# Performance work log

Measured on AMD Instinct MI355X. Metric: run time of the kernel, lower is better.

## Reference

```python
import jax, jax.numpy as jnp
import numpy as np

N_STEPS = 5


def setup_inputs() -> dict:
    key = jax.random.key(0)
    ks = jax.random.split(key, 12)
    B, N, E, D = 4, 2048, 2, 128
    prop_state = jax.random.normal(ks[0], (B, N, D), dtype=jnp.float32)
    A = (jax.random.uniform(ks[1], (B, N, 2 * N * E)) < 0.01).astype(jnp.float32)
    s = 0.02  # init scale from _initialization
    W_in = jax.random.normal(ks[2], (E, D, D), dtype=jnp.float32) * s
    b_in = jax.random.normal(ks[3], (E, D), dtype=jnp.float32) * s
    W_out = jax.random.normal(ks[4], (E, D, D), dtype=jnp.float32) * s
    b_out = jax.random.normal(ks[5], (E, D), dtype=jnp.float32) * s
    W_r = jax.random.normal(ks[6], (3 * D, D), dtype=jnp.float32) * s
    b_r = jax.random.normal(ks[7], (D,), dtype=jnp.float32) * s
    W_z = jax.random.normal(ks[8], (3 * D, D), dtype=jnp.float32) * s
    b_z = jax.random.normal(ks[9], (D,), dtype=jnp.float32) * s
    W_h = jax.random.normal(ks[10], (3 * D, D), dtype=jnp.float32) * s
    b_h = jax.random.normal(ks[11], (D,), dtype=jnp.float32) * s
    return {"prop_state": prop_state, "A": A, "W_in": W_in, "b_in": b_in,
            "W_out": W_out, "b_out": b_out, "W_r": W_r, "b_r": b_r,
            "W_z": W_z, "b_z": b_z, "W_h": W_h, "b_h": b_h}


def _ggnn_forward(prop_state, A, W_in, b_in, W_out, b_out,
                  W_r, b_r, W_z, b_z, W_h, b_h):
    B, N, D = prop_state.shape
    E = W_in.shape[0]
    A_in = A[:, :, : N * E]    # [B, N, N*E]
    A_out = A[:, :, N * E:]    # [B, N, N*E]
    h = prop_state
    for _ in range(N_STEPS):
        # per-edge-type projections, node-major / edge-type-minor ordering
        ins = (jnp.einsum('bnd,edf->bnef', h, W_in) + b_in).reshape(B, N * E, D)
        outs = (jnp.einsum('bnd,edf->bnef', h, W_out) + b_out).reshape(B, N * E, D)
        a_in = jnp.einsum('bnm,bmd->bnd', A_in, ins)    # [B, N, D]
        a_out = jnp.einsum('bnm,bmd->bnd', A_out, outs)  # [B, N, D]
        a = jnp.concatenate([a_in, a_out, h], axis=-1)   # [B, N, 3D]
        r = jax.nn.sigmoid(a @ W_r + b_r)
        z = jax.nn.sigmoid(a @ W_z + b_z)
        joined = jnp.concatenate([a_in, a_out, r * h], axis=-1)
        h_hat = jnp.tanh(joined @ W_h + b_h)
        h = (1.0 - z) * h + z * h_hat
    return h


def reference(prop_state, A, W_in, b_in, W_out, b_out,
              W_r, b_r, W_z, b_z, W_h, b_h):
    return _ggnn_forward(prop_state, A, W_in, b_in, W_out, b_out,
                         W_r, b_r, W_z, b_z, W_h, b_h)
```

## Files before the change

kernel.cpp:

```cpp
#include <hip/hip_runtime.h>
#include <stdint.h>

#define ROWS 8192
#define CAP 64
#define NSTEPS 5
#define ZROW 8192

typedef short bf16x8 __attribute__((ext_vector_type(8)));
typedef float f32x4 __attribute__((ext_vector_type(4)));
typedef float f32x2 __attribute__((ext_vector_type(2)));
typedef unsigned short u16;
typedef unsigned int u32;

__device__ __forceinline__ float bf2f(u16 u){ union{u32 i; float f;} x; x.i=(u32)u<<16; return x.f; }
__device__ __forceinline__ u16 f2bf(float f){ union{float f; u32 i;} x; x.f=f; u32 r = x.i + 0x7fffu + ((x.i>>16)&1u); return (u16)(r>>16); }

#define MFMA __builtin_amdgcn_mfma_f32_16x16x32_bf16
#define SWZ(r, byte) ((byte) ^ (((r)&7)<<4))
#define ZPAD 130


__device__ __forceinline__ float wsel(const float* __restrict__ Wr, const float* __restrict__ Wz,
                                      const float* __restrict__ Wh, int f, int o){
  if (o < 128) return Wr[(size_t)f*128 + o];
  if (o < 256) return Wz[(size_t)f*128 + (o-128)];
  return (f < 256) ? Wh[(size_t)f*128 + (o-256)] : 0.f;
}

__global__ void k_prep(const float* __restrict__ prop, float* __restrict__ hf, u16* __restrict__ hbf,
                       const float* __restrict__ W_in, const float* __restrict__ b_in,
                       const float* __restrict__ W_out, const float* __restrict__ b_out,
                       const float* __restrict__ W_r, const float* __restrict__ W_z,
                       const float* __restrict__ W_h,
                       u16* __restrict__ WfT, float* __restrict__ bv, u16* __restrict__ WhbT)
{
  int bid = blockIdx.x;
  if (bid < 4096){
    int i = bid*256 + threadIdx.x;
    float v = prop[i]; hf[i] = v; hbf[i] = f2bf(v);
    return;
  }
  if (bid == 4096 && threadIdx.x < 128) hbf[(size_t)ZROW*128 + threadIdx.x] = 0;
  int i = (bid-4096)*256 + threadIdx.x;
  if (i < 640*384){
    int k = i/384, o = i - k*384;
    float s;
    if (k >= 512){
      s = wsel(W_r, W_z, W_h, 256 + (k-512), o);
    } else {
      const float* Wrow; int fb;
      if (k < 256){ Wrow = W_in  + (size_t)((k>>7)&1)*16384 + (size_t)(k&127)*128; fb = 0; }
      else { int kk = k-256; Wrow = W_out + (size_t)(kk>>7)*16384 + (size_t)(kk&127)*128; fb = 128; }
      s = 0.f;
#pragma unroll 8
      for (int f=0; f<128; f++) s += Wrow[f] * wsel(W_r, W_z, W_h, fb+f, o);
    }
    WfT[(size_t)o*640 + k] = f2bf(s);
  } else if (i < 640*384 + 4*384){
    int j = i - 640*384; int q = j / 384, o = j - q*384;
    const float* bp = (q < 2) ? (b_in + q*128) : (b_out + (q-2)*128);
    int fb = (q < 2) ? 0 : 128;
    float s = 0.f;
#pragma unroll 8
    for (int f=0; f<128; f++) s += bp[f] * wsel(W_r, W_z, W_h, fb+f, o);
    bv[j] = s;
  } else if (i < 640*384 + 4*384 + 128*128){
    int j = i - (640*384 + 4*384); int kk = j>>7, o = j&127;
    WhbT[(size_t)o*128 + kk] = f2bf(W_h[(size_t)(256+kk)*128 + o]);
  }
}

__global__ void k_csr(const float* __restrict__ A,
                      u16* __restrict__ idx4, int* __restrict__ cnt4)
{
  __shared__ int scnt[4];
  __shared__ int slist[4][CAP];
  int row = blockIdx.x, tid = threadIdx.x;
  if (tid < 4) scnt[tid] = 0;
  __syncthreads();
  const float* ar = A + (size_t)row * 8192;
  int babs = (row>>11)<<11;
  for (int c = tid*4; c < 8192; c += 1024){
    f32x4 v = __builtin_nontemporal_load(reinterpret_cast<const f32x4*>(ar + c));
    float vv[4] = {v.x, v.y, v.z, v.w};
#pragma unroll
    for (int j=0;j<4;j++){
      if (vv[j] != 0.f){
        int m = c + j;
        int lst = ((m>>12)<<1) | (m&1);
        int n = (m & 4095) >> 1;
        int p = atomicAdd(&scnt[lst], 1);
        if (p < CAP) slist[lst][p] = babs | n;
      }
    }
  }
  __syncthreads();
  if (tid < 4) cnt4[(row<<2) + tid] = scnt[tid];
  for (int j = tid; j < 4*CAP; j += 256){
    int l = j>>6, p = j&63;
    int c = scnt[l]; if (c > CAP) c = CAP;
    if (p < c) __builtin_nontemporal_store((u16)slist[l][p],
                  idx4 + (((size_t)(row<<2) + l)<<6) + p);
  }
}

__global__ __launch_bounds__(512, 2) void k_fused(
    const int* __restrict__ cnt4, const u16* __restrict__ idx4,
    const u16* __restrict__ WfT, const float* __restrict__ bv,
    const float* __restrict__ b_r, const float* __restrict__ b_z, const float* __restrict__ b_h,
    const u16* __restrict__ WhbT, float* __restrict__ hf, u16* __restrict__ hbf)
{
  __shared__ u16  X_s[32*512];
  __shared__ u16  rh_s[32*128];
  __shared__ u16  z_s[32*ZPAD];
  __shared__ u16  hh_s[32*ZPAD];
  __shared__ int  cnts[32][4];

  int tid  = threadIdx.x;
  int wave = tid>>6, lane = tid&63, lr = lane&15, lk = lane>>4;

  int d = blockIdx.x;
  int xcd = d & 7, slot = d >> 3;
  int r_blk = ((xcd>>1)<<6) | ((slot<<1) | (xcd&1));
  int m0 = r_blk*32;

  if (tid < 128) cnts[tid>>2][tid&3] = cnt4[((m0 + (tid>>2))<<2) + (tid&3)];
  __syncthreads();

  {
    int base_l = wave*16;
    int cc[16], my[16];
#pragma unroll
    for (int j=0;j<16;j++){
      int l = base_l + j;
      int c = cnts[l>>2][l&3]; if (c > CAP) c = CAP;
      cc[j] = c;
      int lid = ((m0 + (l>>2))<<2) | (l&3);
      my[j] = (lane < c) ? (int)idx4[(((size_t)lid)<<6) + lane] : ZROW;
    }
    int cmax = 0;
#pragma unroll
    for (int j=0;j<16;j++) cmax = max(cmax, cc[j]);

    const u16* hb = hbf + (lane<<1);
    f32x2 a[16];
#pragma unroll
    for (int j=0;j<16;j++) a[j] = (f32x2){0.f, 0.f};

    u32 v[16];
#pragma unroll
    for (int j=0;j<16;j++){
      int n = __builtin_amdgcn_readlane(my[j], 0);
      v[j] = *reinterpret_cast<const u32*>(hb + ((size_t)n<<7));
    }
    for (int i=1; i<cmax; i++){
      u32 vn[16];
#pragma unroll
      for (int j=0;j<16;j++){
        int n = __builtin_amdgcn_readlane(my[j], i);
        vn[j] = *reinterpret_cast<const u32*>(hb + ((size_t)n<<7));
      }
#pragma unroll
      for (int j=0;j<16;j++){
        union{u32 u; float f;} lo, hi;
        lo.u = v[j]<<16; hi.u = v[j] & 0xffff0000u;
        a[j] += (f32x2){lo.f, hi.f};
        v[j] = vn[j];
      }
    }
    if (cmax > 0){
#pragma unroll
      for (int j=0;j<16;j++){
        union{u32 u; float f;} lo, hi;
        lo.u = v[j]<<16; hi.u = v[j] & 0xffff0000u;
        a[j] += (f32x2){lo.f, hi.f};
      }
    }
#pragma unroll
    for (int j=0;j<16;j++){
      int l = base_l + j, rl = l>>2, q = l&3;
      u32 pk = ((u32)f2bf(a[j].y)<<16) | (u32)f2bf(a[j].x);
      *reinterpret_cast<u32*>((char*)X_s + SWZ(rl, rl*1024 + q*256 + lane*4)) = pk;
    }
  }
  __syncthreads();

  int n0 = wave*48;
  f32x4 acc[2][3] = {};
  const u16* Ah = hbf + (size_t)(m0+lr)*128 + lk*8;
  const u16* Bw = WfT + (size_t)(n0+lr)*640 + lk*8;
#pragma unroll
  for (int k=0;k<512;k+=32){
    bf16x8 b0 = *reinterpret_cast<const bf16x8*>(Bw + k);
    bf16x8 b1 = *reinterpret_cast<const bf16x8*>(Bw + 16*640 + k);
    bf16x8 b2 = *reinterpret_cast<const bf16x8*>(Bw + 32*640 + k);
#pragma unroll
    for (int mt=0;mt<2;mt++){
      int row = mt*16 + lr;
      bf16x8 aa = *reinterpret_cast<const bf16x8*>((const char*)X_s + SWZ(row, row*1024 + (k + lk*8)*2));
      acc[mt][0] = MFMA(aa, b0, acc[mt][0], 0,0,0);
      acc[mt][1] = MFMA(aa, b1, acc[mt][1], 0,0,0);
      acc[mt][2] = MFMA(aa, b2, acc[mt][2], 0,0,0);
    }
  }
#pragma unroll
  for (int k=0;k<128;k+=32){
    bf16x8 b0 = *reinterpret_cast<const bf16x8*>(Bw + 512 + k);
    bf16x8 b1 = *reinterpret_cast<const bf16x8*>(Bw + 16*640 + 512 + k);
    bf16x8 b2 = *reinterpret_cast<const bf16x8*>(Bw + 32*640 + 512 + k);
#pragma unroll
    for (int mt=0;mt<2;mt++){
      bf16x8 aa = *reinterpret_cast<const bf16x8*>(Ah + (size_t)mt*16*128 + k);
      acc[mt][0] = MFMA(aa, b0, acc[mt][0], 0,0,0);
      acc[mt][1] = MFMA(aa, b1, acc[mt][1], 0,0,0);
      acc[mt][2] = MFMA(aa, b2, acc[mt][2], 0,0,0);
    }
  }

#pragma unroll
  for (int nt=0;nt<3;nt++){
    int oo = n0 + nt*16 + lr;
    float base = (oo<128) ? b_r[oo] : (oo<256) ? b_z[oo-128] : b_h[oo-256];
    float q0 = bv[oo], q1 = bv[384+oo], q2 = bv[768+oo], q3 = bv[1152+oo];
#pragma unroll
    for (int mt=0;mt<2;mt++){
#pragma unroll
      for (int i2=0;i2<4;i2++){
        int rl = mt*16 + lk*4 + i2;
        float v = acc[mt][nt][i2] + base
                + cnts[rl][0]*q0 + cnts[rl][1]*q1 + cnts[rl][2]*q2 + cnts[rl][3]*q3;
        if (oo < 128){
          float s = 1.f/(1.f + expf(-v));
          float hv = hf[(size_t)(m0+rl)*128 + oo];
          *reinterpret_cast<u16*>((char*)rh_s + SWZ(rl, rl*256 + oo*2)) = f2bf(s*hv);
        } else if (oo < 256){
          float s = 1.f/(1.f + expf(-v));
          z_s[rl*ZPAD + (oo-128)] = (u16)(s*65535.f + 0.5f);
        } else {
          hh_s[rl*ZPAD + (oo-256)] = f2bf(v);
        }
      }
    }
  }
  __syncthreads();

  int c0 = wave*16;
  f32x4 acc2[2] = {};
  const u16* Bh = WhbT + (size_t)(c0+lr)*128 + lk*8;
#pragma unroll
  for (int k=0;k<128;k+=32){
    bf16x8 b = *reinterpret_cast<const bf16x8*>(Bh + k);
#pragma unroll
    for (int mt=0;mt<2;mt++){
      int rr = mt*16 + lr;
      bf16x8 aa = *reinterpret_cast<const bf16x8*>((char*)rh_s + SWZ(rr, rr*256 + (k + lk*8)*2));
      acc2[mt] = MFMA(aa, b, acc2[mt], 0,0,0);
    }
  }

#pragma unroll
  for (int mt=0;mt<2;mt++){
#pragma unroll
    for (int i2=0;i2<4;i2++){
      int rl = mt*16 + lk*4 + i2, col = c0 + lr;
      size_t ix = (size_t)(m0+rl)*128 + col;
      float hhat = tanhf(acc2[mt][i2] + bf2f(hh_s[rl*ZPAD + col]));
      float zz = (float)z_s[rl*ZPAD + col] * (1.f/65535.f);
      float ho = hf[ix];
      float hn = ho + zz*(hhat - ho);
      hf[ix] = hn;
      hbf[ix] = f2bf(hn);
    }
  }
}


extern "C" void kernel_launch(void* const* d_in, const int* in_sizes, int n_in,
                              void* d_out, int out_size, void* d_ws, size_t ws_size,
                              hipStream_t stream)
{
  const float* prop  = (const float*)d_in[0];
  const float* A     = (const float*)d_in[1];
  const float* W_in  = (const float*)d_in[2];
  const float* b_in  = (const float*)d_in[3];
  const float* W_out = (const float*)d_in[4];
  const float* b_out = (const float*)d_in[5];
  const float* W_r   = (const float*)d_in[6];
  const float* b_r   = (const float*)d_in[7];
  const float* W_z   = (const float*)d_in[8];
  const float* b_z   = (const float*)d_in[9];
  const float* W_h   = (const float*)d_in[10];
  const float* b_h   = (const float*)d_in[11];

  char* ws = (char*)d_ws;
  size_t off = 0;
  auto nxt = [&](size_t bytes)->char*{ char* p = ws + off; off += (bytes + 255) & ~(size_t)255; return p; };
  int*   cnt4  = (int*)  nxt((size_t)ROWS*4*4);
  u16*   idx4  = (u16*)  nxt((size_t)ROWS*4*CAP*2);
  u16*   hbf   = (u16*)  nxt((size_t)(ROWS+1)*128*2);
  float* hf    = (float*)nxt((size_t)ROWS*128*4);
  u16*   WfT   = (u16*)  nxt((size_t)384*640*2);
  float* bv    = (float*)nxt((size_t)4*384*4);
  u16*   WhbT  = (u16*)  nxt((size_t)128*128*2);

  int fold_blocks = (640*384 + 4*384 + 128*128 + 255)/256;
  k_prep<<<4096 + fold_blocks, 256, 0, stream>>>(prop, hf, hbf,
      W_in, b_in, W_out, b_out, W_r, W_z, W_h, WfT, bv, WhbT);
  k_csr<<<ROWS, 256, 0, stream>>>(A, idx4, cnt4);

  for (int t=0; t<NSTEPS; t++){
    k_fused<<<ROWS/32, 512, 0, stream>>>(cnt4, idx4, WfT, bv, b_r, b_z, b_h, WhbT, hf, hbf);
  }

  hipMemcpyAsync(d_out, hf, (size_t)ROWS*128*4, hipMemcpyDeviceToDevice, stream);
}
```

Baseline: 290.6 us.

## Gather neighbor rows with 16-byte loads split across four edge groups

The sparse aggregation gather changes from one 4-byte load per lane per neighbor to 16-byte loads. Each quarter-wave now handles a different neighbor, with indices distributed by ds_bpermute, and partial sums are combined by xor shuffles before a packed bf16 convert and a single 16-byte LDS store. This aims to cut the number of memory instructions and loop iterations per row (about four times fewer steps). In exchange it adds shuffle-reduction overhead, and processing the list-groups in blocks of four may reduce memory-level parallelism compared with the earlier 16 independent streams.

```diff
diff --git a/kernel.cpp b/kernel.cpp
--- a/kernel.cpp
+++ b/kernel.cpp
@@ -9,6 +9,7 @@
 typedef short bf16x8 __attribute__((ext_vector_type(8)));
 typedef float f32x4 __attribute__((ext_vector_type(4)));
 typedef float f32x2 __attribute__((ext_vector_type(2)));
+typedef unsigned int u32x4 __attribute__((ext_vector_type(4)));
 typedef unsigned short u16;
 typedef unsigned int u32;
 
@@ -128,59 +129,92 @@
   __syncthreads();
 
   {
-    int base_l = wave*16;
-    int cc[16], my[16];
-#pragma unroll
-    for (int j=0;j<16;j++){
-      int l = base_l + j;
-      int c = cnts[l>>2][l&3]; if (c > CAP) c = CAP;
-      cc[j] = c;
-      int lid = ((m0 + (l>>2))<<2) | (l&3);
-      my[j] = (lane < c) ? (int)idx4[(((size_t)lid)<<6) + lane] : ZROW;
-    }
-    int cmax = 0;
-#pragma unroll
-    for (int j=0;j<16;j++) cmax = max(cmax, cc[j]);
-
-    const u16* hb = hbf + (lane<<1);
-    f32x2 a[16];
-#pragma unroll
-    for (int j=0;j<16;j++) a[j] = (f32x2){0.f, 0.f};
-
-    u32 v[16];
-#pragma unroll
-    for (int j=0;j<16;j++){
-      int n = __builtin_amdgcn_readlane(my[j], 0);
-      v[j] = *reinterpret_cast<const u32*>(hb + ((size_t)n<<7));
-    }
-    for (int i=1; i<cmax; i++){
-      u32 vn[16];
-#pragma unroll
-      for (int j=0;j<16;j++){
-        int n = __builtin_amdgcn_readlane(my[j], i);
-        vn[j] = *reinterpret_cast<const u32*>(hb + ((size_t)n<<7));
-      }
-#pragma unroll
-      for (int j=0;j<16;j++){
-        union{u32 u; float f;} lo, hi;
-        lo.u = v[j]<<16; hi.u = v[j] & 0xffff0000u;
-        a[j] += (f32x2){lo.f, hi.f};
-        v[j] = vn[j];
-      }
-    }
-    if (cmax > 0){
-#pragma unroll
-      for (int j=0;j<16;j++){
-        union{u32 u; float f;} lo, hi;
-        lo.u = v[j]<<16; hi.u = v[j] & 0xffff0000u;
-        a[j] += (f32x2){lo.f, hi.f};
-      }
-    }
-#pragma unroll
-    for (int j=0;j<16;j++){
-      int l = base_l + j, rl = l>>2, q = l&3;
-      u32 pk = ((u32)f2bf(a[j].y)<<16) | (u32)f2bf(a[j].x);
-      *reinterpret_cast<u32*>((char*)X_s + SWZ(rl, rl*1024 + q*256 + lane*4)) = pk;
+    int eg = lane >> 4;
+    int co = (lane & 15) << 4;
+    const char* hb = (const char*)hbf;
+#pragma unroll
+    for (int b=0; b<4; b++){
+      int l0 = wave*16 + b*4;
+      int my[4], cc[4];
+#pragma unroll
+      for (int j=0;j<4;j++){
+        int l = l0 + j;
+        int c = cnts[l>>2][l&3]; if (c > CAP) c = CAP;
+        cc[j] = c;
+        int lid = ((m0 + (l>>2))<<2) | (l&3);
+        my[j] = (lane < c) ? (int)idx4[(((size_t)lid)<<6) + lane] : ZROW;
+      }
+      int cmaxb = max(max(cc[0],cc[1]), max(cc[2],cc[3]));
+      int G = (cmaxb + 3) >> 2;
+
+      f32x2 acc[4][4];
+#pragma unroll
+      for (int j=0;j<4;j++)
+#pragma unroll
+        for (int dd=0;dd<4;dd++) acc[j][dd] = (f32x2){0.f,0.f};
+
+      if (G > 0){
+        u32x4 v0[4];
+        int selb = eg<<2;
+#pragma unroll
+        for (int j=0;j<4;j++){
+          int n = __builtin_amdgcn_ds_bpermute(selb, my[j]);
+          v0[j] = *reinterpret_cast<const u32x4*>(hb + (((size_t)(u32)n)<<8) + co);
+        }
+        for (int i=1; i<G; i++){
+          selb += 16;
+          u32x4 v1[4];
+#pragma unroll
+          for (int j=0;j<4;j++){
+            int n = __builtin_amdgcn_ds_bpermute(selb, my[j]);
+            v1[j] = *reinterpret_cast<const u32x4*>(hb + (((size_t)(u32)n)<<8) + co);
+          }
+#pragma unroll
+          for (int j=0;j<4;j++){
+#pragma unroll
+            for (int dd=0;dd<4;dd++){
+              union{u32 u; float f;} lo, hi;
+              lo.u = v0[j][dd]<<16; hi.u = v0[j][dd] & 0xffff0000u;
+              acc[j][dd] += (f32x2){lo.f, hi.f};
+            }
+            v0[j] = v1[j];
+          }
+        }
+#pragma unroll
+        for (int j=0;j<4;j++)
+#pragma unroll
+          for (int dd=0;dd<4;dd++){
+            union{u32 u; float f;} lo, hi;
+            lo.u = v0[j][dd]<<16; hi.u = v0[j][dd] & 0xffff0000u;
+            acc[j][dd] += (f32x2){lo.f, hi.f};
+          }
+      }
+
+#pragma unroll
+      for (int off=16; off<=32; off<<=1){
+#pragma unroll
+        for (int j=0;j<4;j++)
+#pragma unroll
+          for (int dd=0;dd<4;dd++){
+            acc[j][dd].x += __shfl_xor(acc[j][dd].x, off);
+            acc[j][dd].y += __shfl_xor(acc[j][dd].y, off);
+          }
+      }
+
+      u32 w[4];
+#pragma unroll
+      for (int dd=0;dd<4;dd++){
+        f32x2 t01 = (eg & 1) ? acc[1][dd] : acc[0][dd];
+        f32x2 t23 = (eg & 1) ? acc[3][dd] : acc[2][dd];
+        f32x2 o   = (eg & 2) ? t23 : t01;
+        u32 r;
+        asm("v_cvt_pk_bf16_f32 %0, %1, %2" : "=v"(r) : "v"(o.x), "v"(o.y));
+        w[dd] = r;
+      }
+
+      int l = l0 + eg, rl = l>>2, q = l&3;
+      char* p = (char*)X_s + SWZ(rl, rl*1024 + q*256 + co);
+      *reinterpret_cast<u32x4*>(p) = *reinterpret_cast<u32x4*>(w);
     }
   }
   __syncthreads();
```

After: 408.9 us. 1.41x slower.

## Split sparse gather into separate high-parallelism kernel before dense step

Applied to the files above, without the earlier changes.

The neighbor-sum gather, which ran inside the fused step kernel with only 256 blocks, moves into its own kernel with 2048 blocks of 256 threads, each wave handling 4 lists instead of 16. The result is written to a global bf16 buffer X that the step kernel then reads directly as its MFMA A operand instead of from LDS. The aim is more parallelism and memory-level concurrency for the latency-bound gather. The cost is an extra launch per step and a round trip of X through global memory (about 8 MB per step).

```diff
diff --git a/kernel.cpp b/kernel.cpp
--- a/kernel.cpp
+++ b/kernel.cpp
@@ -104,13 +104,73 @@
   }
 }
 
-__global__ __launch_bounds__(512, 2) void k_fused(
+__global__ __launch_bounds__(256) void k_gather(
     const int* __restrict__ cnt4, const u16* __restrict__ idx4,
+    const u16* __restrict__ hbf, u16* __restrict__ X)
+{
+  int d = blockIdx.x;
+  int xcd = d & 7, slot = d >> 3;
+  int b = ((xcd>>1)<<9) | (slot<<1) | (xcd&1);
+  int m0 = b*4;
+  int wave = threadIdx.x>>6, lane = threadIdx.x&63;
+  int base_l = wave*4;
+
+  int cc[4], my[4];
+#pragma unroll
+  for (int j=0;j<4;j++){
+    int l = base_l + j;
+    int lid = ((m0 + (l>>2))<<2) | (l&3);
+    int c = cnt4[lid]; if (c > CAP) c = CAP;
+    cc[j] = c;
+    my[j] = (lane < c) ? (int)idx4[(((size_t)lid)<<6) + lane] : ZROW;
+  }
+  int cmax = max(max(cc[0],cc[1]), max(cc[2],cc[3]));
+
+  const u16* hb = hbf + (lane<<1);
+  f32x2 a[4] = {};
+  u32 v[4];
+#pragma unroll
+  for (int j=0;j<4;j++){
+    int n = __builtin_amdgcn_readlane(my[j], 0);
+    v[j] = *reinterpret_cast<const u32*>(hb + ((size_t)n<<7));
+  }
+  for (int i=1; i<cmax; i++){
+    u32 vn[4];
+#pragma unroll
+    for (int j=0;j<4;j++){
+      int n = __builtin_amdgcn_readlane(my[j], i);
+      vn[j] = *reinterpret_cast<const u32*>(hb + ((size_t)n<<7));
+    }
+#pragma unroll
+    for (int j=0;j<4;j++){
+      union{u32 u; float f;} lo, hi;
+      lo.u = v[j]<<16; hi.u = v[j] & 0xffff0000u;
+      a[j] += (f32x2){lo.f, hi.f};
+      v[j] = vn[j];
+    }
+  }
+  if (cmax > 0){
+#pragma unroll
+    for (int j=0;j<4;j++){
+      union{u32 u; float f;} lo, hi;
+      lo.u = v[j]<<16; hi.u = v[j] & 0xffff0000u;
+      a[j] += (f32x2){lo.f, hi.f};
+    }
+  }
+#pragma unroll
+  for (int j=0;j<4;j++){
+    int l = base_l + j, rl = l>>2, q = l&3;
+    u32 pk = ((u32)f2bf(a[j].y)<<16) | (u32)f2bf(a[j].x);
+    *reinterpret_cast<u32*>(X + (size_t)(m0+rl)*512 + (q<<7) + (lane<<1)) = pk;
+  }
+}
+
+__global__ __launch_bounds__(512, 2) void k_step(
+    const int* __restrict__ cnt4, const u16* __restrict__ X,
     const u16* __restrict__ WfT, const float* __restrict__ bv,
     const float* __restrict__ b_r, const float* __restrict__ b_z, const float* __restrict__ b_h,
     const u16* __restrict__ WhbT, float* __restrict__ hf, u16* __restrict__ hbf)
 {
-  __shared__ u16  X_s[32*512];
   __shared__ u16  rh_s[32*128];
   __shared__ u16  z_s[32*ZPAD];
   __shared__ u16  hh_s[32*ZPAD];
@@ -127,66 +187,9 @@
   if (tid < 128) cnts[tid>>2][tid&3] = cnt4[((m0 + (tid>>2))<<2) + (tid&3)];
   __syncthreads();
 
-  {
-    int base_l = wave*16;
-    int cc[16], my[16];
-#pragma unroll
-    for (int j=0;j<16;j++){
-      int l = base_l + j;
-      int c = cnts[l>>2][l&3]; if (c > CAP) c = CAP;
-      cc[j] = c;
-      int lid = ((m0 + (l>>2))<<2) | (l&3);
-      my[j] = (lane < c) ? (int)idx4[(((size_t)lid)<<6) + lane] : ZROW;
-    }
-    int cmax = 0;
-#pragma unroll
-    for (int j=0;j<16;j++) cmax = max(cmax, cc[j]);
-
-    const u16* hb = hbf + (lane<<1);
-    f32x2 a[16];
-#pragma unroll
-    for (int j=0;j<16;j++) a[j] = (f32x2){0.f, 0.f};
-
-    u32 v[16];
-#pragma unroll
-    for (int j=0;j<16;j++){
-      int n = __builtin_amdgcn_readlane(my[j], 0);
-      v[j] = *reinterpret_cast<const u32*>(hb + ((size_t)n<<7));
-    }
-    for (int i=1; i<cmax; i++){
-      u32 vn[16];
-#pragma unroll
-      for (int j=0;j<16;j++){
-        int n = __builtin_amdgcn_readlane(my[j], i);
-        vn[j] = *reinterpret_cast<const u32*>(hb + ((size_t)n<<7));
-      }
-#pragma unroll
-      for (int j=0;j<16;j++){
-        union{u32 u; float f;} lo, hi;
-        lo.u = v[j]<<16; hi.u = v[j] & 0xffff0000u;
-        a[j] += (f32x2){lo.f, hi.f};
-        v[j] = vn[j];
-      }
-    }
-    if (cmax > 0){
-#pragma unroll
-      for (int j=0;j<16;j++){
-        union{u32 u; float f;} lo, hi;
-        lo.u = v[j]<<16; hi.u = v[j] & 0xffff0000u;
-        a[j] += (f32x2){lo.f, hi.f};
-      }
-    }
-#pragma unroll
-    for (int j=0;j<16;j++){
-      int l = base_l + j, rl = l>>2, q = l&3;
-      u32 pk = ((u32)f2bf(a[j].y)<<16) | (u32)f2bf(a[j].x);
-      *reinterpret_cast<u32*>((char*)X_s + SWZ(rl, rl*1024 + q*256 + lane*4)) = pk;
-    }
-  }
-  __syncthreads();
-
   int n0 = wave*48;
   f32x4 acc[2][3] = {};
+  const u16* Ax = X   + (size_t)(m0+lr)*512 + lk*8;
   const u16* Ah = hbf + (size_t)(m0+lr)*128 + lk*8;
   const u16* Bw = WfT + (size_t)(n0+lr)*640 + lk*8;
 #pragma unroll
@@ -196,8 +199,7 @@
     bf16x8 b2 = *reinterpret_cast<const bf16x8*>(Bw + 32*640 + k);
 #pragma unroll
     for (int mt=0;mt<2;mt++){
-      int row = mt*16 + lr;
-      bf16x8 aa = *reinterpret_cast<const bf16x8*>((const char*)X_s + SWZ(row, row*1024 + (k + lk*8)*2));
+      bf16x8 aa = *reinterpret_cast<const bf16x8*>(Ax + (size_t)mt*16*512 + k);
       acc[mt][0] = MFMA(aa, b0, acc[mt][0], 0,0,0);
       acc[mt][1] = MFMA(aa, b1, acc[mt][1], 0,0,0);
       acc[mt][2] = MFMA(aa, b2, acc[mt][2], 0,0,0);
@@ -299,6 +301,7 @@
   u16*   idx4  = (u16*)  nxt((size_t)ROWS*4*CAP*2);
   u16*   hbf   = (u16*)  nxt((size_t)(ROWS+1)*128*2);
   float* hf    = (float*)nxt((size_t)ROWS*128*4);
+  u16*   X     = (u16*)  nxt((size_t)ROWS*512*2);
   u16*   WfT   = (u16*)  nxt((size_t)384*640*2);
   float* bv    = (float*)nxt((size_t)4*384*4);
   u16*   WhbT  = (u16*)  nxt((size_t)128*128*2);
@@ -309,7 +312,8 @@
   k_csr<<<ROWS, 256, 0, stream>>>(A, idx4, cnt4);
 
   for (int t=0; t<NSTEPS; t++){
-    k_fused<<<ROWS/32, 512, 0, stream>>>(cnt4, idx4, WfT, bv, b_r, b_z, b_h, WhbT, hf, hbf);
+    k_gather<<<ROWS/4, 256, 0, stream>>>(cnt4, idx4, hbf, X);
+    k_step  <<<ROWS/32, 512, 0, stream>>>(cnt4, X, WfT, bv, b_r, b_z, b_h, WhbT, hf, hbf);
   }
 
   hipMemcpyAsync(d_out, hf, (size_t)ROWS*128*4, hipMemcpyDeviceToDevice, stream);
```

Result: slower. 318.1 us (+9.5%).
